# Kernel optimization log

Measured on AMD Instinct MI355X. Metric: run time of the kernel, lower is better.

## Reference

```python
import jax, jax.numpy as jnp
import numpy as np

N_NODES = 50000
N_EDGES = 800000
IN_CH = 128
OUT_CH = 64


def setup_inputs() -> dict:
    key = jax.random.key(0)
    ks = jax.random.split(key, 8)
    cat = IN_CH + OUT_CH
    scale = 1.0 / np.sqrt(cat)
    return {
        "x": jax.random.normal(ks[0], (N_NODES, IN_CH), dtype=jnp.float32),
        "edge_index": jax.random.randint(ks[1], (2, N_EDGES), 0, N_NODES, dtype=jnp.int64),
        "edge_weight": jax.random.uniform(ks[2], (N_EDGES,), dtype=jnp.float32),
        "hidden_state": jax.random.normal(ks[3], (N_NODES, OUT_CH), dtype=jnp.float32),
        "W_z": jax.random.normal(ks[4], (cat, OUT_CH), dtype=jnp.float32) * scale,
        "b_z": jnp.zeros((OUT_CH,), dtype=jnp.float32),
        "W_r": jax.random.normal(ks[5], (cat, OUT_CH), dtype=jnp.float32) * scale,
        "b_r": jnp.zeros((OUT_CH,), dtype=jnp.float32),
        "W_h": jax.random.normal(ks[6], (cat, OUT_CH), dtype=jnp.float32) * scale,
        "b_h": jnp.zeros((OUT_CH,), dtype=jnp.float32),
    }


def _gcn_norm(row, col, w, num_nodes):
    # PyG GCNConv normalization with self-loops (fill_value=1):
    # norm_e = deg[row]^-1/2 * w_e * deg[col]^-1/2 over loop-augmented edges
    loops = jnp.arange(num_nodes, dtype=row.dtype)
    row = jnp.concatenate([row, loops])
    col = jnp.concatenate([col, loops])
    w = jnp.concatenate([w, jnp.ones((num_nodes,), dtype=w.dtype)])
    deg = jax.ops.segment_sum(w, col, num_segments=num_nodes)
    dinv = jnp.where(deg > 0, jax.lax.rsqrt(deg), 0.0)
    norm = dinv[row] * w * dinv[col]
    return row, col, norm


def _gcn_conv(x_cat, W, b, row, col, norm, num_nodes):
    h = x_cat @ W                                   # (N, out)
    msg = h[row] * norm[:, None]                    # (E+N, out) gather + scale
    out = jax.ops.segment_sum(msg, col, num_segments=num_nodes)
    return out + b


def reference(x, edge_index, edge_weight, hidden_state,
              W_z, b_z, W_r, b_r, W_h, b_h):
    n = x.shape[0]
    row, col, norm = _gcn_norm(edge_index[0], edge_index[1], edge_weight, n)
    xh = jnp.concatenate([x, hidden_state], axis=1)
    z = jax.nn.sigmoid(_gcn_conv(xh, W_z, b_z, row, col, norm, n))
    r = jax.nn.sigmoid(_gcn_conv(xh, W_r, b_r, row, col, norm, n))
    xrh = jnp.concatenate([x, r * hidden_state], axis=1)
    h_cand = jnp.tanh(_gcn_conv(xrh, W_h, b_h, row, col, norm, n))
    return z * hidden_state + (1.0 - z) * h_cand
```

## Files before the change

### kernel.cpp

```cpp
#include <hip/hip_runtime.h>
#include <hip/hip_bf16.h>
#include <cstdint>
#include <cstddef>

#define IN_CH   128
#define OUT_CH  64
#define CAT_CH  192
#define ALD     56
#define BLD     40

typedef short bf16x8 __attribute__((ext_vector_type(8)));
typedef float f32x4  __attribute__((ext_vector_type(4)));
typedef float f32x2  __attribute__((ext_vector_type(2)));
typedef unsigned long long u64;
typedef unsigned int u32;

__device__ __forceinline__ float sigmoidf_(float x) { return 1.f / (1.f + __expf(-x)); }

__device__ __forceinline__ unsigned short f2bf(float f) {
    u32 u = __float_as_uint(f);
    u32 r = (u + 0x7fffu + ((u >> 16) & 1u)) >> 16;
    return (unsigned short)r;
}
__device__ __forceinline__ u32 pk2bf(float a, float b) {
    return (u32)f2bf(a) | ((u32)f2bf(b) << 16);
}
__device__ __forceinline__ float bflo(u32 v) { return __uint_as_float(v << 16); }
__device__ __forceinline__ float bfhi(u32 v) { return __uint_as_float(v & 0xffff0000u); }

__device__ __forceinline__ unsigned char f2e4m3(float f) {
    u32 p = __builtin_amdgcn_cvt_pk_fp8_f32(f, f, 0, false);
    return (unsigned char)p;
}
template <bool HI>
__device__ __forceinline__ f32x2 fp8pk(u32 v) {
    return __builtin_amdgcn_cvt_pk_f32_fp8((int)v, HI);
}

__device__ __forceinline__ u32 xcc_id() {
    u32 v;
    asm("s_getreg_b32 %0, hwreg(HW_REG_XCC_ID)" : "=s"(v));
    return v & 7u;
}

__device__ __forceinline__ int load_col(const void* ei, int i, int E, int f) {
    return f ? ((const int*)ei)[E + i] : (int)((const long long*)ei)[E + i];
}
__device__ __forceinline__ int load_row(const void* ei, int i, int E, int f) {
    return f ? ((const int*)ei)[i] : (int)((const long long*)ei)[i];
}

__global__ void prep_kernel(int4* __restrict__ zdst, int n16,
                            const unsigned int* __restrict__ ei, int* __restrict__ flag,
                            const float* __restrict__ Wz, const float* __restrict__ Wr,
                            const float* __restrict__ Wh,
                            unsigned short* __restrict__ Bzrt, unsigned short* __restrict__ Wht,
                            int gZ) {
    int b = blockIdx.x, t = threadIdx.x;
    if (b < gZ) {
        int i = b * 256 + t;
        if (i < n16) zdst[i] = make_int4(0, 0, 0, 0);
    } else if (b == gZ) {
        if (t < 64) {
            unsigned int v = ei[(t << 1) + 1];
            unsigned long long bl = __ballot(v != 0u);
            if (t == 0) *flag = (bl != 0ull) ? 1 : 0;
        }
    } else {
        int i = (b - gZ - 1) * 256 + t;
        if (i < 192 * CAT_CH) {
            int col = i / CAT_CH, k = i % CAT_CH;
            if (col < 128) {
                float v = (col < 64) ? Wz[k * 64 + col] : Wr[k * 64 + (col - 64)];
                Bzrt[col * CAT_CH + k] = f2bf(v);
            } else {
                Wht[(col - 128) * CAT_CH + k] = f2bf(Wh[k * 64 + (col - 128)]);
            }
        }
    }
}

template <int TN, int OUT, bool A1F32>
__device__ __forceinline__ void gemm_body(
    unsigned short* __restrict__ As ,
    unsigned short* __restrict__ Bs ,
    int blk, const float* __restrict__ A0, int a0w,
    const void* __restrict__ A1, int a1w,
    const unsigned short* __restrict__ Bt, int bOff, int K,
    const float* __restrict__ Cacc, void* __restrict__ Cout, int nrows)
{
    const int t = threadIdx.x, lane = t & 63, wave = t >> 6;
    const int rowBase = blk * 128;

    f32x4 acc[2][TN / 16];
#pragma unroll
    for (int rf = 0; rf < 2; rf++)
#pragma unroll
        for (int cf = 0; cf < TN / 16; cf++) acc[rf][cf] = (f32x4){0.f, 0.f, 0.f, 0.f};

    const int srow = t >> 1, half = t & 1;
    int arow = rowBase + srow;
    if (arow >= nrows) arow = nrows - 1;

    for (int k0 = 0; k0 < K; k0 += 32) {
        __syncthreads();
        {
            int kk = k0 + half * 16;
            u32 pk[8];
            if (kk < a0w) {
                const float* src = A0 + (size_t)arow * a0w + kk;
#pragma unroll
                for (int q = 0; q < 4; q++) {
                    float4 v = *(const float4*)(src + q * 4);
                    pk[q * 2]     = pk2bf(v.x, v.y);
                    pk[q * 2 + 1] = pk2bf(v.z, v.w);
                }
            } else if (A1F32) {
                const float* src = (const float*)A1 + (size_t)arow * a1w + (kk - a0w);
#pragma unroll
                for (int q = 0; q < 4; q++) {
                    float4 v = *(const float4*)(src + q * 4);
                    pk[q * 2]     = pk2bf(v.x, v.y);
                    pk[q * 2 + 1] = pk2bf(v.z, v.w);
                }
            } else {
                const unsigned short* src =
                    (const unsigned short*)A1 + (size_t)arow * a1w + (kk - a0w);
                int4 v0 = *(const int4*)src;
                int4 v1 = *(const int4*)(src + 8);
                pk[0] = v0.x; pk[1] = v0.y; pk[2] = v0.z; pk[3] = v0.w;
                pk[4] = v1.x; pk[5] = v1.y; pk[6] = v1.z; pk[7] = v1.w;
            }
            *(int4*)&As[srow * ALD + half * 16]     = make_int4(pk[0], pk[1], pk[2], pk[3]);
            *(int4*)&As[srow * ALD + half * 16 + 8] = make_int4(pk[4], pk[5], pk[6], pk[7]);
        }
#pragma unroll
        for (int idx = t * 8; idx < TN * 32; idx += 256 * 8) {
            int col = idx >> 5, kk = idx & 31;
            *(int4*)&Bs[col * BLD + kk] =
                *(const int4*)&Bt[(size_t)col * CAT_CH + bOff + k0 + kk];
        }
        __syncthreads();

        const int rbase = wave * 32;
        const int koff = (lane >> 4) * 8;
        bf16x8 a0 = *(const bf16x8*)&As[(rbase + (lane & 15)) * ALD + koff];
        bf16x8 a1 = *(const bf16x8*)&As[(rbase + 16 + (lane & 15)) * ALD + koff];
#pragma unroll
        for (int cf = 0; cf < TN / 16; cf++) {
            bf16x8 b = *(const bf16x8*)&Bs[(cf * 16 + (lane & 15)) * BLD + koff];
            acc[0][cf] = __builtin_amdgcn_mfma_f32_16x16x32_bf16(a0, b, acc[0][cf], 0, 0, 0);
            acc[1][cf] = __builtin_amdgcn_mfma_f32_16x16x32_bf16(a1, b, acc[1][cf], 0, 0, 0);
        }
    }

#pragma unroll
    for (int rf = 0; rf < 2; rf++)
#pragma unroll
        for (int cf = 0; cf < TN / 16; cf++) {
            int row0 = rowBase + wave * 32 + rf * 16 + (lane >> 4) * 4;
            int col  = cf * 16 + (lane & 15);
#pragma unroll
            for (int r = 0; r < 4; r++) {
                int row = row0 + r;
                if (row < nrows) {
                    float v = acc[rf][cf][r];
                    if (Cacc) v += Cacc[(size_t)row * TN + col];
                    if (OUT == 1)
                        ((unsigned char*)Cout)[(size_t)row * TN + col] = f2e4m3(v);
                    else if (OUT == 2)
                        ((float*)Cout)[(size_t)row * TN + col] = v;
                    else
                        ((unsigned short*)Cout)[(size_t)row * TN + col] = f2bf(v);
                }
            }
        }
}

__global__ __launch_bounds__(256) void work1_kernel(
    const float* __restrict__ x, const float* __restrict__ hidden,
    const unsigned short* __restrict__ Bzrt, const unsigned short* __restrict__ Wht,
    unsigned char* __restrict__ Hzr8, float* __restrict__ Hh32,
    const void* __restrict__ ei, const float* __restrict__ ew,
    u64* __restrict__ packed8, u32* __restrict__ rank,
    const int* __restrict__ flag, int E, int N, int gM)
{
    __shared__ unsigned short As[128 * ALD];
    __shared__ unsigned short Bs[128 * BLD];

    const int blk = blockIdx.x;
    int role, idx;
    if (blk < 3 * gM) { role = blk % 3; idx = blk / 3; }
    else              { role = 2;       idx = gM + (blk - 3 * gM); }

    if (role == 0) {
        gemm_body<128, 1, true>(As, Bs, idx, x, 128, (const void*)hidden, 64,
                                Bzrt, 0, 192, nullptr, (void*)Hzr8, N);
    } else if (role == 1) {
        gemm_body<64, 2, false>(As, Bs, idx, x, 128, nullptr, 0,
                                Wht, 0, 128, nullptr, (void*)Hh32, N);
    } else {
        int i0 = (idx * 256 + threadIdx.x) * 4;
        if (i0 >= E) return;
        const u32 shard = xcc_id();
        u64* __restrict__ shp = packed8 + (size_t)shard * N;
        int f = *flag;
        u32 rk[4];
#pragma unroll
        for (int k = 0; k < 4; k++) {
            int i = i0 + k;
            if (i < E) {
                int c = load_col(ei, i, E, f);
                u32 wq = __float2uint_rn(ew[i] * 1048576.0f);
                u64 old = __hip_atomic_fetch_add(&shp[c], (1ull << 32) | (u64)wq,
                                                 __ATOMIC_RELAXED,
                                                 __HIP_MEMORY_SCOPE_WORKGROUP);
                rk[k] = (shard << 28) | (u32)(old >> 32);
            }
        }
#pragma unroll
        for (int k = 0; k < 4; k++)
            if (i0 + k < E) rank[i0 + k] = rk[k];
    }
}

__global__ __launch_bounds__(256) void gemm2b_kernel(
    const unsigned short* __restrict__ RHb, const unsigned short* __restrict__ Wht,
    const float* __restrict__ Hh32, unsigned short* __restrict__ Hhb, int N)
{
    __shared__ unsigned short As[128 * ALD];
    __shared__ unsigned short Bs[64 * BLD];
    gemm_body<64, 0, false>(As, Bs, blockIdx.x, nullptr, 0, (const void*)RHb, 64,
                            Wht, 128, 64, Hh32, (void*)Hhb, N);
}

__global__ __launch_bounds__(256) void scan1_kernel(const u64* __restrict__ packed8,
                                                    float* __restrict__ dinv,
                                                    u32* __restrict__ shoff,
                                                    int* __restrict__ starts,
                                                    int* __restrict__ bsum, int n) {
    __shared__ int s[256];
    int i = blockIdx.x * 256 + threadIdx.x;
    int v = 0;
    if (i < n) {
        u32 run = 0, wsum = 0;
#pragma unroll
        for (int sh = 0; sh < 8; sh++) {
            u64 p = packed8[(size_t)sh * n + i];
            shoff[(size_t)sh * n + i] = run;
            run  += (u32)(p >> 32);
            wsum += (u32)p;
        }
        float ws = (float)wsum * (1.0f / 1048576.0f);
        dinv[i] = rsqrtf(1.0f + ws);
        v = (int)run;
    }
    s[threadIdx.x] = v;
    __syncthreads();
#pragma unroll
    for (int d = 1; d < 256; d <<= 1) {
        int t = (threadIdx.x >= d) ? s[threadIdx.x - d] : 0;
        __syncthreads();
        s[threadIdx.x] += t;
        __syncthreads();
    }
    if (i < n) starts[i] = s[threadIdx.x] - v;
    if (threadIdx.x == 255) bsum[blockIdx.x] = s[255];
}

__global__ __launch_bounds__(256) void scan2_kernel(int* __restrict__ bsum, int nb) {
    __shared__ int s[256];
    int t = threadIdx.x;
    int v = (t < nb) ? bsum[t] : 0;
    s[t] = v;
    __syncthreads();
#pragma unroll
    for (int d = 1; d < 256; d <<= 1) {
        int u = (t >= d) ? s[t - d] : 0;
        __syncthreads();
        s[t] += u;
        __syncthreads();
    }
    if (t < nb) bsum[t] = s[t] - v;
}

__global__ void scan3_kernel(int* __restrict__ starts, const int* __restrict__ boff,
                             int n, int E) {
    int i = blockIdx.x * blockDim.x + threadIdx.x;
    if (i == 0) starts[n] = E;
    if (i < n) starts[i] += boff[blockIdx.x];
}

__global__ void scatter2_kernel(const void* __restrict__ ei, const float* __restrict__ w,
                                const float* __restrict__ dinv, const int* __restrict__ starts,
                                const u32* __restrict__ shoff, const u32* __restrict__ rank,
                                u64* __restrict__ pairs, const int* __restrict__ flag,
                                int E, int N) {
    int i0 = (blockIdx.x * blockDim.x + threadIdx.x) * 4;
    if (i0 >= E) return;
    int f = *flag;
    int r[4], c[4];
#pragma unroll
    for (int k = 0; k < 4; k++) {
        int i = i0 + k;
        if (i < E) { r[k] = load_row(ei, i, E, f); c[k] = load_col(ei, i, E, f); }
    }
#pragma unroll
    for (int k = 0; k < 4; k++) {
        int i = i0 + k;
        if (i < E) {
            float nm = dinv[r[k]] * w[i] * dinv[c[k]];
            u32 rk = rank[i];
            u32 sh = rk >> 28, rks = rk & 0x0fffffffu;
            int pos = starts[c[k]] + (int)shoff[(size_t)sh * N + c[k]] + (int)rks;
            pairs[pos] = ((u64)__float_as_uint(nm) << 32) | (u32)(r[k] << 7);
        }
    }
}

__global__ __launch_bounds__(256) void spmm_zr_kernel(
    const unsigned char* __restrict__ H8, const u64* __restrict__ pairs,
    const int* __restrict__ starts, const float* __restrict__ dinv,
    const float* __restrict__ hidden, const float* __restrict__ bz,
    const float* __restrict__ br, float* __restrict__ Z,
    unsigned short* __restrict__ RHb, int N)
{
    int node = (blockIdx.x * 256 + threadIdx.x) >> 6;
    if (node >= N) return;
    const int lane = threadIdx.x & 63;
    const int sub = lane & 31, half = lane >> 5;
    int s = starts[node], e = starts[node + 1];
    float d = dinv[node], d2 = d * d;

    float a0 = 0.f, a1 = 0.f, a2 = 0.f, a3 = 0.f;
    if (half == 0) {
        u32 sv = *(const u32*)&H8[(size_t)node * 128 + sub * 4];
        f32x2 s01 = fp8pk<false>(sv), s23 = fp8pk<true>(sv);
        a0 = s01.x * d2; a1 = s01.y * d2; a2 = s23.x * d2; a3 = s23.y * d2;
    }

    int j = s;
    int full = s + ((e - s) & ~15);
    for (; j < full; j += 16) {
        u32 hv[8]; float nm[8];
#pragma unroll
        for (int k = 0; k < 8; k++) {
            u64 p = pairs[j + k * 2 + half];
            nm[k] = __uint_as_float((u32)(p >> 32));
            hv[k] = *(const u32*)&H8[(size_t)(u32)p + sub * 4];
        }
#pragma unroll
        for (int k = 0; k < 8; k++) {
            f32x2 h01 = fp8pk<false>(hv[k]), h23 = fp8pk<true>(hv[k]);
            a0 = fmaf(h01.x, nm[k], a0); a1 = fmaf(h01.y, nm[k], a1);
            a2 = fmaf(h23.x, nm[k], a2); a3 = fmaf(h23.y, nm[k], a3);
        }
    }
    if (j < e) {
        u32 hv[8]; float nm[8];
#pragma unroll
        for (int k = 0; k < 8; k++) {
            int jj = j + k * 2 + half;
            u64 p = pairs[(jj < e) ? jj : (e - 1)];
            nm[k] = (jj < e) ? __uint_as_float((u32)(p >> 32)) : 0.f;
            hv[k] = *(const u32*)&H8[(size_t)(u32)p + sub * 4];
        }
#pragma unroll
        for (int k = 0; k < 8; k++) {
            f32x2 h01 = fp8pk<false>(hv[k]), h23 = fp8pk<true>(hv[k]);
            a0 = fmaf(h01.x, nm[k], a0); a1 = fmaf(h01.y, nm[k], a1);
            a2 = fmaf(h23.x, nm[k], a2); a3 = fmaf(h23.y, nm[k], a3);
        }
    }

    a0 += __shfl_xor(a0, 32, 64);
    a1 += __shfl_xor(a1, 32, 64);
    a2 += __shfl_xor(a2, 32, 64);
    a3 += __shfl_xor(a3, 32, 64);

    if (half == 0) {
        if (sub < 16) {
            int c = sub * 4;
            float4 b4 = *(const float4*)&bz[c];
            float4 o = { sigmoidf_(a0 + b4.x), sigmoidf_(a1 + b4.y),
                         sigmoidf_(a2 + b4.z), sigmoidf_(a3 + b4.w) };
            *(float4*)&Z[(size_t)node * 64 + c] = o;
        } else {
            int c = (sub - 16) * 4;
            float4 b4 = *(const float4*)&br[c];
            float4 hid = *(const float4*)&hidden[(size_t)node * 64 + c];
            float r0 = sigmoidf_(a0 + b4.x) * hid.x;
            float r1 = sigmoidf_(a1 + b4.y) * hid.y;
            float r2 = sigmoidf_(a2 + b4.z) * hid.z;
            float r3 = sigmoidf_(a3 + b4.w) * hid.w;
            ushort4 o = { f2bf(r0), f2bf(r1), f2bf(r2), f2bf(r3) };
            *(ushort4*)&RHb[(size_t)node * 64 + c] = o;
        }
    }
}

__global__ __launch_bounds__(256) void spmm_h_kernel(
    const unsigned short* __restrict__ H, const u64* __restrict__ pairs,
    const int* __restrict__ starts, const float* __restrict__ dinv,
    const float* __restrict__ hidden, const float* __restrict__ bh,
    const float* __restrict__ Z, float* __restrict__ out, int N)
{
    int node = (blockIdx.x * 256 + threadIdx.x) >> 6;
    if (node >= N) return;
    const int lane = threadIdx.x & 63;
    const int sub = lane & 31, half = lane >> 5;
    const unsigned char* Hb = (const unsigned char*)H;
    int s = starts[node], e = starts[node + 1];
    float d = dinv[node], d2 = d * d;

    float ax = 0.f, ay = 0.f;
    if (half == 0) {
        u32 sv = *(const u32*)&Hb[(size_t)node * 128 + sub * 4];
        ax = bflo(sv) * d2; ay = bfhi(sv) * d2;
    }

    int j = s;
    int full = s + ((e - s) & ~15);
    for (; j < full; j += 16) {
        u32 hv[8]; float nm[8];
#pragma unroll
        for (int k = 0; k < 8; k++) {
            u64 p = pairs[j + k * 2 + half];
            nm[k] = __uint_as_float((u32)(p >> 32));
            hv[k] = *(const u32*)&Hb[(size_t)(u32)p + sub * 4];
        }
#pragma unroll
        for (int k = 0; k < 8; k++) {
            ax = fmaf(bflo(hv[k]), nm[k], ax);
            ay = fmaf(bfhi(hv[k]), nm[k], ay);
        }
    }
    if (j < e) {
        u32 hv[8]; float nm[8];
#pragma unroll
        for (int k = 0; k < 8; k++) {
            int jj = j + k * 2 + half;
            u64 p = pairs[(jj < e) ? jj : (e - 1)];
            nm[k] = (jj < e) ? __uint_as_float((u32)(p >> 32)) : 0.f;
            hv[k] = *(const u32*)&Hb[(size_t)(u32)p + sub * 4];
        }
#pragma unroll
        for (int k = 0; k < 8; k++) {
            ax = fmaf(bflo(hv[k]), nm[k], ax);
            ay = fmaf(bfhi(hv[k]), nm[k], ay);
        }
    }

    ax += __shfl_xor(ax, 32, 64);
    ay += __shfl_xor(ay, 32, 64);

    if (half == 0) {
        int c = sub * 2;
        size_t idx = (size_t)node * 64 + c;
        float2 hid = *(const float2*)&hidden[idx];
        float2 z   = *(const float2*)&Z[idx];
        float hc0 = tanhf(ax + bh[c]);
        float hc1 = tanhf(ay + bh[c + 1]);
        float2 o = { z.x * hid.x + (1.f - z.x) * hc0,
                     z.y * hid.y + (1.f - z.y) * hc1 };
        *(float2*)&out[idx] = o;
    }
}

extern "C" void kernel_launch(void* const* d_in, const int* in_sizes, int n_in,
                              void* d_out, int out_size, void* d_ws, size_t ws_size,
                              hipStream_t stream) {
    const float* x      = (const float*)d_in[0];
    const void*  eidx   = d_in[1];
    const float* ew     = (const float*)d_in[2];
    const float* hidden = (const float*)d_in[3];
    const float* Wz     = (const float*)d_in[4];
    const float* bz     = (const float*)d_in[5];
    const float* Wr     = (const float*)d_in[6];
    const float* br     = (const float*)d_in[7];
    const float* Wh     = (const float*)d_in[8];
    const float* bh     = (const float*)d_in[9];
    float* out = (float*)d_out;

    const int E = in_sizes[2];
    const int N = in_sizes[3] / OUT_CH;

    char* base = (char*)d_ws;
    size_t off = 0;
    auto carve = [&](size_t bytes) -> char* {
        char* p = base + off;
        off = (off + bytes + 255) & ~(size_t)255;
        return p;
    };
    u64*   packed8 = (u64*) carve((size_t)N * 8 * 8);
    u32*   shoff   = (u32*) carve((size_t)N * 8 * 4);
    u32*   rank    = (u32*) carve((size_t)E * 4);
    float* dinv    = (float*)carve((size_t)N * 4);
    int*   starts  = (int*)  carve((size_t)(N + 1) * 4);
    int*   bsum    = (int*)  carve(256 * 4);
    u64*   pairs   = (u64*)  carve((size_t)E * 8);
    unsigned char*  Hzr8 = (unsigned char*)carve((size_t)N * 128);
    unsigned short* RHb  = (unsigned short*)carve((size_t)N * 64 * 2);
    unsigned short* Hhb  = (unsigned short*)carve((size_t)N * 64 * 2);
    float* Hh32 = (float*)carve((size_t)N * 64 * 4);
    float* Z    = (float*)carve((size_t)N * 64 * 4);
    unsigned short* Bzrt = (unsigned short*)carve((size_t)128 * CAT_CH * 2);
    unsigned short* Wht  = (unsigned short*)carve((size_t)64 * CAT_CH * 2);
    int* flag = (int*)carve(4);
    if (off > ws_size) return;

    const int B256 = 256;
    const int gE4 = (E + 1023) / 1024;
    const int gN = (N + B256 - 1) / B256;
    const int gM = (N + 127) / 128;
    const int gW = (N + 3) / 4;
    const int n16 = N * 4;
    const int gZ = (n16 + B256 - 1) / B256;
    const int gP = (192 * CAT_CH + 255) / 256;

    hipLaunchKernelGGL(prep_kernel, dim3(gZ + 1 + gP), dim3(B256), 0, stream,
                       (int4*)packed8, n16, (const unsigned int*)eidx, flag,
                       Wz, Wr, Wh, Bzrt, Wht, gZ);

    hipLaunchKernelGGL(work1_kernel, dim3(2 * gM + gE4), dim3(B256), 0, stream,
                       x, hidden, Bzrt, Wht, Hzr8, Hh32,
                       eidx, ew, packed8, rank, flag, E, N, gM);

    hipLaunchKernelGGL(scan1_kernel, dim3(gN), dim3(B256), 0, stream,
                       packed8, dinv, shoff, starts, bsum, N);
    hipLaunchKernelGGL(scan2_kernel, dim3(1), dim3(B256), 0, stream, bsum, gN);
    hipLaunchKernelGGL(scan3_kernel, dim3(gN), dim3(B256), 0, stream, starts, bsum, N, E);

    hipLaunchKernelGGL(scatter2_kernel, dim3(gE4), dim3(B256), 0, stream,
                       eidx, ew, dinv, starts, shoff, rank, pairs, flag, E, N);

    hipLaunchKernelGGL(spmm_zr_kernel, dim3(gW), dim3(B256), 0, stream,
                       Hzr8, pairs, starts, dinv, hidden, bz, br, Z, RHb, N);

    hipLaunchKernelGGL(gemm2b_kernel, dim3(gM), dim3(B256), 0, stream,
                       RHb, Wht, Hh32, Hhb, N);

    hipLaunchKernelGGL(spmm_h_kernel, dim3(gW), dim3(B256), 0, stream,
                       Hhb, pairs, starts, dinv, hidden, bh, Z, out, N);
}
```

Measured before the change: 164.3 us.

## Use nontemporal loads/stores for streaming data and fuse block-offset scan kernels

Replaces plain global loads and stores of streamed-once data (edge indices, weights, ranks, CSR pairs, GEMM inputs and outputs) with nontemporal builtins, so they are less likely to evict reused data such as the gathered feature rows from cache. Separately, it merges the single-block scan2 and the scan3 offset-add into one kernel where each block reduces the preceding block sums itself, removing one launch and its dependency. This adds redundant per-block reductions, and the nontemporal hints may hurt if written data like pairs and Hzr8 is read back soon after.

```diff
diff --git a/kernel.cpp b/kernel.cpp
--- a/kernel.cpp
+++ b/kernel.cpp
@@ -12,6 +12,7 @@
 typedef short bf16x8 __attribute__((ext_vector_type(8)));
 typedef float f32x4  __attribute__((ext_vector_type(4)));
 typedef float f32x2  __attribute__((ext_vector_type(2)));
+typedef int   i32x4  __attribute__((ext_vector_type(4)));
 typedef unsigned long long u64;
 typedef unsigned int u32;
 
@@ -43,11 +44,19 @@
     return v & 7u;
 }
 
-__device__ __forceinline__ int load_col(const void* ei, int i, int E, int f) {
-    return f ? ((const int*)ei)[E + i] : (int)((const long long*)ei)[E + i];
-}
-__device__ __forceinline__ int load_row(const void* ei, int i, int E, int f) {
-    return f ? ((const int*)ei)[i] : (int)((const long long*)ei)[i];
+__device__ __forceinline__ int ntl_i32(const int* p)        { return __builtin_nontemporal_load(p); }
+__device__ __forceinline__ long long ntl_i64(const long long* p) { return __builtin_nontemporal_load(p); }
+__device__ __forceinline__ float ntl_f32(const float* p)    { return __builtin_nontemporal_load(p); }
+__device__ __forceinline__ u32  ntl_u32(const u32* p)       { return __builtin_nontemporal_load(p); }
+__device__ __forceinline__ u64  ntl_u64(const u64* p)       { return __builtin_nontemporal_load(p); }
+__device__ __forceinline__ f32x4 ntl_f32x4(const float* p)  { return __builtin_nontemporal_load((const f32x4*)p); }
+__device__ __forceinline__ i32x4 ntl_i32x4(const void* p)   { return __builtin_nontemporal_load((const i32x4*)p); }
+
+__device__ __forceinline__ int load_col_nt(const void* ei, int i, int E, int f) {
+    return f ? ntl_i32((const int*)ei + E + i) : (int)ntl_i64((const long long*)ei + E + i);
+}
+__device__ __forceinline__ int load_row_nt(const void* ei, int i, int E, int f) {
+    return f ? ntl_i32((const int*)ei + i) : (int)ntl_i64((const long long*)ei + i);
 }
 
 __global__ void prep_kernel(int4* __restrict__ zdst, int n16,
@@ -111,25 +120,25 @@
                 const float* src = A0 + (size_t)arow * a0w + kk;
 #pragma unroll
                 for (int q = 0; q < 4; q++) {
-                    float4 v = *(const float4*)(src + q * 4);
-                    pk[q * 2]     = pk2bf(v.x, v.y);
-                    pk[q * 2 + 1] = pk2bf(v.z, v.w);
+                    f32x4 v = ntl_f32x4(src + q * 4);
+                    pk[q * 2]     = pk2bf(v[0], v[1]);
+                    pk[q * 2 + 1] = pk2bf(v[2], v[3]);
                 }
             } else if (A1F32) {
                 const float* src = (const float*)A1 + (size_t)arow * a1w + (kk - a0w);
 #pragma unroll
                 for (int q = 0; q < 4; q++) {
-                    float4 v = *(const float4*)(src + q * 4);
-                    pk[q * 2]     = pk2bf(v.x, v.y);
-                    pk[q * 2 + 1] = pk2bf(v.z, v.w);
+                    f32x4 v = ntl_f32x4(src + q * 4);
+                    pk[q * 2]     = pk2bf(v[0], v[1]);
+                    pk[q * 2 + 1] = pk2bf(v[2], v[3]);
                 }
             } else {
                 const unsigned short* src =
                     (const unsigned short*)A1 + (size_t)arow * a1w + (kk - a0w);
-                int4 v0 = *(const int4*)src;
-                int4 v1 = *(const int4*)(src + 8);
-                pk[0] = v0.x; pk[1] = v0.y; pk[2] = v0.z; pk[3] = v0.w;
-                pk[4] = v1.x; pk[5] = v1.y; pk[6] = v1.z; pk[7] = v1.w;
+                i32x4 v0 = ntl_i32x4(src);
+                i32x4 v1 = ntl_i32x4(src + 8);
+                pk[0] = v0[0]; pk[1] = v0[1]; pk[2] = v0[2]; pk[3] = v0[3];
+                pk[4] = v1[0]; pk[5] = v1[1]; pk[6] = v1[2]; pk[7] = v1[3];
             }
             *(int4*)&As[srow * ALD + half * 16]     = make_int4(pk[0], pk[1], pk[2], pk[3]);
             *(int4*)&As[srow * ALD + half * 16 + 8] = make_int4(pk[4], pk[5], pk[6], pk[7]);
@@ -165,11 +174,13 @@
                 int row = row0 + r;
                 if (row < nrows) {
                     float v = acc[rf][cf][r];
-                    if (Cacc) v += Cacc[(size_t)row * TN + col];
+                    if (Cacc) v += ntl_f32(&Cacc[(size_t)row * TN + col]);
                     if (OUT == 1)
-                        ((unsigned char*)Cout)[(size_t)row * TN + col] = f2e4m3(v);
+                        __builtin_nontemporal_store(f2e4m3(v),
+                            (unsigned char*)Cout + (size_t)row * TN + col);
                     else if (OUT == 2)
-                        ((float*)Cout)[(size_t)row * TN + col] = v;
+                        __builtin_nontemporal_store(v,
+                            (float*)Cout + (size_t)row * TN + col);
                     else
                         ((unsigned short*)Cout)[(size_t)row * TN + col] = f2bf(v);
                 }
@@ -210,8 +221,8 @@
         for (int k = 0; k < 4; k++) {
             int i = i0 + k;
             if (i < E) {
-                int c = load_col(ei, i, E, f);
-                u32 wq = __float2uint_rn(ew[i] * 1048576.0f);
+                int c = load_col_nt(ei, i, E, f);
+                u32 wq = __float2uint_rn(ntl_f32(&ew[i]) * 1048576.0f);
                 u64 old = __hip_atomic_fetch_add(&shp[c], (1ull << 32) | (u64)wq,
                                                  __ATOMIC_RELAXED,
                                                  __HIP_MEMORY_SCOPE_WORKGROUP);
@@ -220,7 +231,7 @@
         }
 #pragma unroll
         for (int k = 0; k < 4; k++)
-            if (i0 + k < E) rank[i0 + k] = rk[k];
+            if (i0 + k < E) __builtin_nontemporal_store(rk[k], &rank[i0 + k]);
     }
 }
 
@@ -268,27 +279,22 @@
     if (threadIdx.x == 255) bsum[blockIdx.x] = s[255];
 }
 
-__global__ __launch_bounds__(256) void scan2_kernel(int* __restrict__ bsum, int nb) {
+__global__ __launch_bounds__(256) void scan3_kernel(int* __restrict__ starts,
+                                                    const int* __restrict__ bsum,
+                                                    int n, int E, int nb) {
     __shared__ int s[256];
     int t = threadIdx.x;
-    int v = (t < nb) ? bsum[t] : 0;
-    s[t] = v;
+    s[t] = (t < nb && t < (int)blockIdx.x) ? bsum[t] : 0;
     __syncthreads();
 #pragma unroll
-    for (int d = 1; d < 256; d <<= 1) {
-        int u = (t >= d) ? s[t - d] : 0;
+    for (int d = 128; d > 0; d >>= 1) {
+        if (t < d) s[t] += s[t + d];
         __syncthreads();
-        s[t] += u;
-        __syncthreads();
-    }
-    if (t < nb) bsum[t] = s[t] - v;
-}
-
-__global__ void scan3_kernel(int* __restrict__ starts, const int* __restrict__ boff,
-                             int n, int E) {
-    int i = blockIdx.x * blockDim.x + threadIdx.x;
-    if (i == 0) starts[n] = E;
-    if (i < n) starts[i] += boff[blockIdx.x];
+    }
+    int boff = s[0];
+    int i = blockIdx.x * 256 + t;
+    if (i < n) starts[i] += boff;
+    if (i == n) starts[n] = E;
 }
 
 __global__ void scatter2_kernel(const void* __restrict__ ei, const float* __restrict__ w,
@@ -303,17 +309,18 @@
 #pragma unroll
     for (int k = 0; k < 4; k++) {
         int i = i0 + k;
-        if (i < E) { r[k] = load_row(ei, i, E, f); c[k] = load_col(ei, i, E, f); }
+        if (i < E) { r[k] = load_row_nt(ei, i, E, f); c[k] = load_col_nt(ei, i, E, f); }
     }
 #pragma unroll
     for (int k = 0; k < 4; k++) {
         int i = i0 + k;
         if (i < E) {
-            float nm = dinv[r[k]] * w[i] * dinv[c[k]];
-            u32 rk = rank[i];
+            float nm = dinv[r[k]] * ntl_f32(&w[i]) * dinv[c[k]];
+            u32 rk = ntl_u32(&rank[i]);
             u32 sh = rk >> 28, rks = rk & 0x0fffffffu;
             int pos = starts[c[k]] + (int)shoff[(size_t)sh * N + c[k]] + (int)rks;
-            pairs[pos] = ((u64)__float_as_uint(nm) << 32) | (u32)(r[k] << 7);
+            __builtin_nontemporal_store(
+                ((u64)__float_as_uint(nm) << 32) | (u32)(r[k] << 7), &pairs[pos]);
         }
     }
 }
@@ -345,7 +352,7 @@
         u32 hv[8]; float nm[8];
 #pragma unroll
         for (int k = 0; k < 8; k++) {
-            u64 p = pairs[j + k * 2 + half];
+            u64 p = ntl_u64(&pairs[j + k * 2 + half]);
             nm[k] = __uint_as_float((u32)(p >> 32));
             hv[k] = *(const u32*)&H8[(size_t)(u32)p + sub * 4];
         }
@@ -425,7 +432,7 @@
         u32 hv[8]; float nm[8];
 #pragma unroll
         for (int k = 0; k < 8; k++) {
-            u64 p = pairs[j + k * 2 + half];
+            u64 p = ntl_u64(&pairs[j + k * 2 + half]);
             nm[k] = __uint_as_float((u32)(p >> 32));
             hv[k] = *(const u32*)&Hb[(size_t)(u32)p + sub * 4];
         }
@@ -528,8 +535,8 @@
 
     hipLaunchKernelGGL(scan1_kernel, dim3(gN), dim3(B256), 0, stream,
                        packed8, dinv, shoff, starts, bsum, N);
-    hipLaunchKernelGGL(scan2_kernel, dim3(1), dim3(B256), 0, stream, bsum, gN);
-    hipLaunchKernelGGL(scan3_kernel, dim3(gN), dim3(B256), 0, stream, starts, bsum, N, E);
+    hipLaunchKernelGGL(scan3_kernel, dim3(gN), dim3(B256), 0, stream,
+                       starts, bsum, N, E, gN);
 
     hipLaunchKernelGGL(scatter2_kernel, dim3(gE4), dim3(B256), 0, stream,
                        eidx, ew, dinv, starts, shoff, rank, pairs, flag, E, N);
```

Result: slower. 204.8 us (+24.7%).
